# Kernel tuning notes

Measured on AMD Instinct MI355X. Metric: run time of the kernel, lower is better.

The kernel has to match this reference:

```python
import jax, jax.numpy as jnp
import numpy as np

EPS = 1e-6
B, C, T, F, K = 8, 128, 128, 512, 64


def conv1x1(x, w, b):
    # x: [B,C,H,W], w: [O,C], b: [O]
    return jnp.einsum('bcij,oc->boij', x, w) + b[None, :, None, None]


def rmsnorm(x, g):
    # RMSNorm over channel dim with per-channel gain
    return x * jax.lax.rsqrt(jnp.mean(x * x, axis=1, keepdims=True) + EPS) * g[None, :, None, None]


def swiglu(x, wi, bi, wo, bo):
    h = conv1x1(x, wi, bi)
    a, g = jnp.split(h, 2, axis=1)
    return conv1x1(a * jax.nn.silu(g), wo, bo)


def setup_inputs() -> dict:
    key = jax.random.key(0)
    ks = jax.random.split(key, 16)
    s = 1.0 / np.sqrt(C)
    # soft band-partition basis [K, F]: Gaussian bumps over frequency
    centers = np.linspace(0, F - 1, K)[:, None]
    freqs = np.arange(F)[None, :]
    basis = np.exp(-((freqs - centers) / (F / K)) ** 2).astype(np.float32)
    inp = {
        'latent': jax.random.normal(ks[0], (B, C, T, K), jnp.float32),
        'side': jax.random.normal(ks[1], (B, C, T, F), jnp.float32),
        'expansion_basis': jnp.asarray(basis),
        'lp_gamma': jnp.ones((C,), jnp.float32),
        'lp_w': jax.random.normal(ks[2], (C, C), jnp.float32) * s,
        'lp_b': jnp.zeros((C,), jnp.float32),
        'qn_gamma': jnp.ones((C,), jnp.float32),
        'qmlp_in_w': jax.random.normal(ks[3], (2 * C, C), jnp.float32) * s,
        'qmlp_in_b': jnp.zeros((2 * C,), jnp.float32),
        'qmlp_out_w': jax.random.normal(ks[4], (C, C), jnp.float32) * s,
        'qmlp_out_b': jnp.zeros((C,), jnp.float32),
        'q_w': jax.random.normal(ks[5], (C, C), jnp.float32) * s,
        'q_b': jnp.zeros((C,), jnp.float32),
        'k_w': jax.random.normal(ks[6], (C, C), jnp.float32) * s,
        'k_b': jnp.zeros((C,), jnp.float32),
        'v_w': jax.random.normal(ks[7], (C, C), jnp.float32) * s,
        'v_b': jnp.zeros((C,), jnp.float32),
        'o_w': jax.random.normal(ks[8], (C, C), jnp.float32) * s,
        'o_b': jnp.zeros((C,), jnp.float32),
        'ffn_gamma': jnp.ones((C,), jnp.float32),
        'ffn_in_w': jax.random.normal(ks[9], (2 * C, C), jnp.float32) * s,
        'ffn_in_b': jnp.zeros((2 * C,), jnp.float32),
        'ffn_out_w': jax.random.normal(ks[10], (C, C), jnp.float32) * s,
        'ffn_out_b': jnp.zeros((C,), jnp.float32),
        'score_scale': jnp.asarray(1.0 / np.sqrt(C), jnp.float32),
        'prior_scale': jnp.asarray(1.0, jnp.float32),
        'query_skip_scale': jnp.asarray(1.0, jnp.float32),
    }
    return inp


def reference(latent, side, expansion_basis, lp_gamma, lp_w, lp_b, qn_gamma,
              qmlp_in_w, qmlp_in_b, qmlp_out_w, qmlp_out_b,
              q_w, q_b, k_w, k_b, v_w, v_b, o_w, o_b,
              ffn_gamma, ffn_in_w, ffn_in_b, ffn_out_w, ffn_out_b,
              score_scale, prior_scale, query_skip_scale):
    # latent_pre: RMSNorm -> 1x1 conv -> SiLU   (latent: [B,C,T,K])
    latent_h = jax.nn.silu(conv1x1(rmsnorm(latent, lp_gamma), lp_w, lp_b))
    # adaptive query from full-resolution side path (side: [B,C,T,F])
    query_h = swiglu(rmsnorm(side, qn_gamma), qmlp_in_w, qmlp_in_b, qmlp_out_w, qmlp_out_b)
    # q/k/v projections (1x1 convs)
    q = conv1x1(query_h, q_w, q_b)      # [B,C,T,F]
    k = conv1x1(latent_h, k_w, k_b)     # [B,C,T,K]
    v = conv1x1(latent_h, v_w, v_b)     # [B,C,T,K]
    # per-frame cross-attention scores [B,T,F,K]
    scores = jnp.einsum('bctf,bctk->btfk', q, k) * score_scale
    # learned band-prior bias: expansion_basis [K,F] -> [F,K]
    scores = scores + expansion_basis.T[None, None] * prior_scale
    weights = jax.nn.softmax(scores, axis=-1)  # normalize_band_scores, mode='softmax'
    attended = jnp.einsum('btfk,bctk->bctf', weights, v)
    hidden = conv1x1(attended, o_w, o_b) + query_h * query_skip_scale
    hidden = hidden + swiglu(rmsnorm(hidden, ffn_gamma), ffn_in_w, ffn_in_b, ffn_out_w, ffn_out_b)
    return hidden  # [B,C,T,F]
```

## Files before the change

kernel.cpp:

```cpp
#include <hip/hip_runtime.h>

static constexpr int Cc = 128, Tt = 128, Ff = 512, Kk = 64;
static constexpr int SR = 136;
static constexpr int PR = 88;

typedef __bf16 bf16x8 __attribute__((ext_vector_type(8)));
typedef __bf16 bf16x4 __attribute__((ext_vector_type(4)));
typedef float f32x16 __attribute__((ext_vector_type(16)));
typedef float f32x4 __attribute__((ext_vector_type(4)));

__device__ __forceinline__ f32x16 z16() {
  f32x16 v;
#pragma unroll
  for (int i = 0; i < 16; ++i) v[i] = 0.f;
  return v;
}
__device__ __forceinline__ f32x4 z4() {
  f32x4 v;
#pragma unroll
  for (int i = 0; i < 4; ++i) v[i] = 0.f;
  return v;
}
__device__ __forceinline__ float silu_f(float x) { return x / (1.0f + __expf(-x)); }

__device__ __forceinline__ void rmsnorm_lds(const __bf16* __restrict__ src,
                                            __bf16* __restrict__ dst,
                                            const float* __restrict__ gamma,
                                            float* sPart, float* sr, int tid) {
  {
    int f = tid >> 2, s2 = tid & 3;
    const __bf16* p = src + f * SR + s2 * 32;
    float sum = 0.f;
#pragma unroll
    for (int k = 0; k < 4; ++k) {
      bf16x8 v = *(const bf16x8*)(p + k * 8);
#pragma unroll
      for (int j = 0; j < 8; ++j) { float x = (float)v[j]; sum += x * x; }
    }
    sPart[f * 4 + s2] = sum;
  }
  __syncthreads();
  if (tid < 64) {
    float s = sPart[tid * 4] + sPart[tid * 4 + 1] + sPart[tid * 4 + 2] + sPart[tid * 4 + 3];
    sr[tid] = rsqrtf(s * (1.f / 128.f) + 1e-6f);
  }
  __syncthreads();
#pragma unroll
  for (int i = 0; i < 32; ++i) {
    int idx = i * 256 + tid;
    int f = idx >> 7, c = idx & 127;
    dst[f * SR + c] = (__bf16)((float)src[f * SR + c] * sr[f] * gamma[c]);
  }
}

template <typename EPI>
__device__ __forceinline__ void unit_std(const __bf16* __restrict__ X,
                                         const __bf16* __restrict__ W,
                                         int lane, int wave, EPI epi) {
  const int h = lane >> 5, ol = lane & 31;
  const int p = wave >> 1, mt = wave & 1;
  const int oA = p * 64 + ol;
  bf16x8 B0[8], B1[8];
#pragma unroll
  for (int s = 0; s < 8; ++s) {
    B0[s] = *(const bf16x8*)(W + (size_t)oA * 128 + s * 16 + h * 8);
    B1[s] = *(const bf16x8*)(W + (size_t)(oA + 32) * 128 + s * 16 + h * 8);
  }
  f32x16 a0 = z16(), a1 = z16();
  const __bf16* Ar = X + (mt * 32 + ol) * SR + h * 8;
#pragma unroll
  for (int s = 0; s < 8; ++s) {
    bf16x8 Af = *(const bf16x8*)(Ar + s * 16);
    a0 = __builtin_amdgcn_mfma_f32_32x32x16_bf16(Af, B0[s], a0, 0, 0, 0);
    a1 = __builtin_amdgcn_mfma_f32_32x32x16_bf16(Af, B1[s], a1, 0, 0, 0);
  }
  epi(a0, 0);
  epi(a1, 1);
}

struct PrepArgs {
  const float* src[9];
  int n[9];
};
__global__ __launch_bounds__(256) void prep_kernel(PrepArgs pa, __bf16* __restrict__ dst) {
  int off = 0;
  for (int m = 0; m < 9; ++m) {
    const float* s = pa.src[m];
    int n = pa.n[m];
    for (int i = blockIdx.x * 256 + threadIdx.x; i < n; i += gridDim.x * 256)
      dst[off + i] = (__bf16)s[i];
    off += n;
  }
}

__global__ __launch_bounds__(256, 2)
void kv_kernel(const float* __restrict__ latent, const float* __restrict__ lp_gamma,
               const float* __restrict__ lp_b, const float* __restrict__ k_b,
               const float* __restrict__ v_b,
               const __bf16* __restrict__ w_lp, const __bf16* __restrict__ w_k,
               const __bf16* __restrict__ w_v,
               __bf16* __restrict__ kbuf, __bf16* __restrict__ vbuf) {
  __shared__ __align__(16) __bf16 S0[64 * SR];
  __shared__ __align__(16) __bf16 S1[64 * SR];
  __shared__ float sPart[256];
  __shared__ float sr[64];
  const int tid = threadIdx.x;
  const int lane = tid & 63, wave = tid >> 6;
  const int h = lane >> 5, ol = lane & 31;
  const int fr = blockIdx.x;
  const int b = fr >> 7, t = fr & 127;
  const size_t lbase = ((size_t)b * Cc * Tt + t) * Kk;

#pragma unroll
  for (int i = 0; i < 32; ++i) {
    int idx = i * 256 + tid;
    int c = idx >> 6, kk = idx & 63;
    S0[kk * SR + c] = (__bf16)latent[lbase + (size_t)c * Tt * Kk + kk];
  }
  __syncthreads();
  rmsnorm_lds(S0, S0, lp_gamma, sPart, sr, tid);
  __syncthreads();

  unit_std(S0, w_lp, lane, wave, [&](const f32x16& a, int tix) {
    int o = (wave >> 1) * 64 + tix * 32 + ol;
    int mt = wave & 1;
    float bb = lp_b[o];
#pragma unroll
    for (int r = 0; r < 16; ++r) {
      int f = mt * 32 + (r & 3) + 8 * (r >> 2) + 4 * h;
      S1[f * SR + o] = (__bf16)silu_f(a[r] + bb);
    }
  });
  __syncthreads();

  __bf16* kb = kbuf + (size_t)fr * 8192;
  unit_std(S1, w_k, lane, wave, [&](const f32x16& a, int tix) {
    int o = (wave >> 1) * 64 + tix * 32 + ol;
    int mt = wave & 1;
    float bb = k_b[o];
#pragma unroll
    for (int r = 0; r < 16; ++r) {
      int kkr = mt * 32 + (r & 3) + 8 * (r >> 2) + 4 * h;
      kb[kkr * 128 + o] = (__bf16)(a[r] + bb);
    }
  });
  __bf16* vb = vbuf + (size_t)fr * 8192;
  unit_std(S1, w_v, lane, wave, [&](const f32x16& a, int tix) {
    int o = (wave >> 1) * 64 + tix * 32 + ol;
    int mt = wave & 1;
    float bb = v_b[o];
    __bf16* vbo = vb + (size_t)o * 64 + mt * 32;
#pragma unroll
    for (int q = 0; q < 4; ++q) {
      bf16x4 pk;
      pk[0] = (__bf16)(a[4 * q + 0] + bb);
      pk[1] = (__bf16)(a[4 * q + 1] + bb);
      pk[2] = (__bf16)(a[4 * q + 2] + bb);
      pk[3] = (__bf16)(a[4 * q + 3] + bb);
      *(bf16x4*)(vbo + 8 * q + 4 * h) = pk;
    }
  });
}

__global__ __launch_bounds__(256, 2)
void main_kernel(const float* __restrict__ side, const float* __restrict__ basis,
                 const float* __restrict__ qn_gamma,
                 const float* __restrict__ qin_b, const float* __restrict__ qout_b,
                 const float* __restrict__ q_b, const float* __restrict__ o_b,
                 const float* __restrict__ ffn_gamma,
                 const float* __restrict__ fin_b, const float* __restrict__ fout_b,
                 const __bf16* __restrict__ w_qin, const __bf16* __restrict__ w_qout,
                 const __bf16* __restrict__ w_q, const __bf16* __restrict__ w_o,
                 const __bf16* __restrict__ w_fin, const __bf16* __restrict__ w_fout,
                 const __bf16* __restrict__ kbuf, const __bf16* __restrict__ vbuf,
                 const float* __restrict__ p_sscale, const float* __restrict__ p_pscale,
                 const float* __restrict__ p_skip, float* __restrict__ out) {
  __shared__ __align__(16) __bf16 S0[64 * SR];
  __shared__ __align__(16) __bf16 S1[64 * SR];
  __shared__ __align__(16) __bf16 S2[64 * SR];
  __shared__ __align__(16) __bf16 PM[64 * PR];
  __shared__ float sPart[256];
  __shared__ float sr[64];
  const int tid = threadIdx.x;
  const int lane = tid & 63, wave = tid >> 6;
  const int h = lane >> 5, ol = lane & 31;
  const int bid = blockIdx.x;
  const int fr = bid >> 3, tile = bid & 7;
  const int b = fr >> 7, t = fr & 127;
  const int fbase = tile * 64;
  const size_t sbase = ((size_t)b * Cc * Tt + t) * Ff + fbase;
  const float sscale = *p_sscale, pscale = *p_pscale, skip = *p_skip;
  const __bf16* kfr = kbuf + (size_t)fr * 8192;
  const __bf16* vfr = vbuf + (size_t)fr * 8192;

#pragma unroll
  for (int i = 0; i < 32; ++i) {
    int idx = i * 256 + tid;
    int c = idx >> 6, f = idx & 63;
    S0[f * SR + c] = (__bf16)side[sbase + (size_t)c * Tt * Ff + f];
  }
  __syncthreads();
  rmsnorm_lds(S0, S0, qn_gamma, sPart, sr, tid);
  __syncthreads();

  {
    float sg[2][16];
    unit_std(S0, w_qin + 128 * 128, lane, wave, [&](const f32x16& a, int tix) {
      int o = (wave >> 1) * 64 + tix * 32 + ol;
      float bb = qin_b[128 + o];
#pragma unroll
      for (int r = 0; r < 16; ++r) sg[tix][r] = silu_f(a[r] + bb);
    });
    unit_std(S0, w_qin, lane, wave, [&](const f32x16& a, int tix) {
      int o = (wave >> 1) * 64 + tix * 32 + ol;
      int mt = wave & 1;
      float bb = qin_b[o];
#pragma unroll
      for (int r = 0; r < 16; ++r) {
        int f = mt * 32 + (r & 3) + 8 * (r >> 2) + 4 * h;
        S1[f * SR + o] = (__bf16)((a[r] + bb) * sg[tix][r]);
      }
    });
  }
  __syncthreads();

  unit_std(S1, w_qout, lane, wave, [&](const f32x16& a, int tix) {
    int o = (wave >> 1) * 64 + tix * 32 + ol;
    int mt = wave & 1;
    float bb = qout_b[o];
#pragma unroll
    for (int r = 0; r < 16; ++r) {
      int f = mt * 32 + (r & 3) + 8 * (r >> 2) + 4 * h;
      S2[f * SR + o] = (__bf16)(a[r] + bb);
    }
  });
  __syncthreads();

  unit_std(S2, w_q, lane, wave, [&](const f32x16& a, int tix) {
    int o = (wave >> 1) * 64 + tix * 32 + ol;
    int mt = wave & 1;
    float bb = q_b[o];
#pragma unroll
    for (int r = 0; r < 16; ++r) {
      int f = mt * 32 + (r & 3) + 8 * (r >> 2) + 4 * h;
      S0[f * SR + o] = (__bf16)(a[r] + bb);
    }
  });
  __syncthreads();

  {
    const int q4 = lane >> 4, li = lane & 15;
    const int fw = wave * 16;
    f32x4 acc[4] = {z4(), z4(), z4(), z4()};
    const __bf16* Ar = S0 + (fw + li) * SR + q4 * 8;
    const __bf16* Kr = kfr + li * 128 + q4 * 8;
#pragma unroll
    for (int s = 0; s < 4; ++s) {
      bf16x8 Af = *(const bf16x8*)(Ar + s * 32);
#pragma unroll
      for (int nt = 0; nt < 4; ++nt) {
        bf16x8 Bf = *(const bf16x8*)(Kr + nt * (16 * 128) + s * 32);
        acc[nt] = __builtin_amdgcn_mfma_f32_16x16x32_bf16(Af, Bf, acc[nt], 0, 0, 0);
      }
    }
    float sc[4][4];
#pragma unroll
    for (int nt = 0; nt < 4; ++nt)
#pragma unroll
      for (int r = 0; r < 4; ++r) {
        int kk = 16 * nt + li;
        int f = fw + 4 * q4 + r;
        sc[nt][r] = acc[nt][r] * sscale + pscale * basis[(size_t)kk * Ff + fbase + f];
      }
#pragma unroll
    for (int r = 0; r < 4; ++r) {
      float m = fmaxf(fmaxf(sc[0][r], sc[1][r]), fmaxf(sc[2][r], sc[3][r]));
      m = fmaxf(m, __shfl_xor(m, 1));
      m = fmaxf(m, __shfl_xor(m, 2));
      m = fmaxf(m, __shfl_xor(m, 4));
      m = fmaxf(m, __shfl_xor(m, 8));
      float e[4], ssum = 0.f;
#pragma unroll
      for (int nt = 0; nt < 4; ++nt) { e[nt] = __expf(sc[nt][r] - m); ssum += e[nt]; }
      ssum += __shfl_xor(ssum, 1);
      ssum += __shfl_xor(ssum, 2);
      ssum += __shfl_xor(ssum, 4);
      ssum += __shfl_xor(ssum, 8);
      float inv = 1.f / ssum;
      int f = fw + 4 * q4 + r;
#pragma unroll
      for (int nt = 0; nt < 4; ++nt) PM[f * PR + 16 * nt + li] = (__bf16)(e[nt] * inv);
    }
  }
  __syncthreads();

  {
    const __bf16* Vr = vfr + (size_t)(wave * 32 + ol) * 64 + h * 8;
    bf16x8 Bv[4];
#pragma unroll
    for (int s = 0; s < 4; ++s) Bv[s] = *(const bf16x8*)(Vr + s * 16);
    f32x16 a0 = z16(), a1 = z16();
    const __bf16* Ar = PM + ol * PR + h * 8;
#pragma unroll
    for (int s = 0; s < 4; ++s) {
      bf16x8 A0 = *(const bf16x8*)(Ar + s * 16);
      bf16x8 A1 = *(const bf16x8*)(Ar + 32 * PR + s * 16);
      a0 = __builtin_amdgcn_mfma_f32_32x32x16_bf16(A0, Bv[s], a0, 0, 0, 0);
      a1 = __builtin_amdgcn_mfma_f32_32x32x16_bf16(A1, Bv[s], a1, 0, 0, 0);
    }
    int c = wave * 32 + ol;
#pragma unroll
    for (int r = 0; r < 16; ++r) {
      int fl = (r & 3) + 8 * (r >> 2) + 4 * h;
      S1[fl * SR + c] = (__bf16)a0[r];
      S1[(32 + fl) * SR + c] = (__bf16)a1[r];
    }
  }
  __syncthreads();

  unit_std(S1, w_o, lane, wave, [&](const f32x16& a, int tix) {
    int o = (wave >> 1) * 64 + tix * 32 + ol;
    int mt = wave & 1;
    float bb = o_b[o];
#pragma unroll
    for (int r = 0; r < 16; ++r) {
      int f = mt * 32 + (r & 3) + 8 * (r >> 2) + 4 * h;
      S0[f * SR + o] = (__bf16)(a[r] + bb + skip * (float)S2[f * SR + o]);
    }
  });
  __syncthreads();

  rmsnorm_lds(S0, S2, ffn_gamma, sPart, sr, tid);
  __syncthreads();

  {
    float sg[2][16];
    unit_std(S2, w_fin + 128 * 128, lane, wave, [&](const f32x16& a, int tix) {
      int o = (wave >> 1) * 64 + tix * 32 + ol;
      float bb = fin_b[128 + o];
#pragma unroll
      for (int r = 0; r < 16; ++r) sg[tix][r] = silu_f(a[r] + bb);
    });
    unit_std(S2, w_fin, lane, wave, [&](const f32x16& a, int tix) {
      int o = (wave >> 1) * 64 + tix * 32 + ol;
      int mt = wave & 1;
      float bb = fin_b[o];
#pragma unroll
      for (int r = 0; r < 16; ++r) {
        int f = mt * 32 + (r & 3) + 8 * (r >> 2) + 4 * h;
        S1[f * SR + o] = (__bf16)((a[r] + bb) * sg[tix][r]);
      }
    });
  }
  __syncthreads();

  unit_std(S1, w_fout, lane, wave, [&](const f32x16& a, int tix) {
    int o = (wave >> 1) * 64 + tix * 32 + ol;
    int mt = wave & 1;
    float bb = fout_b[o];
    float* op = out + (((size_t)b * 128 + o) * 128 + t) * 512 + fbase + mt * 32;
#pragma unroll
    for (int q = 0; q < 4; ++q) {
      int f0l = 8 * q + 4 * h;
      float4 v;
      v.x = a[4 * q + 0] + bb + (float)S0[(mt * 32 + f0l + 0) * SR + o];
      v.y = a[4 * q + 1] + bb + (float)S0[(mt * 32 + f0l + 1) * SR + o];
      v.z = a[4 * q + 2] + bb + (float)S0[(mt * 32 + f0l + 2) * SR + o];
      v.w = a[4 * q + 3] + bb + (float)S0[(mt * 32 + f0l + 3) * SR + o];
      *(float4*)(op + f0l) = v;
    }
  });
}

extern "C" void kernel_launch(void* const* d_in, const int* in_sizes, int n_in,
                              void* d_out, int out_size, void* d_ws, size_t ws_size,
                              hipStream_t stream) {
  const float* latent    = (const float*)d_in[0];
  const float* side      = (const float*)d_in[1];
  const float* basis     = (const float*)d_in[2];
  const float* lp_gamma  = (const float*)d_in[3];
  const float* lp_w      = (const float*)d_in[4];
  const float* lp_b      = (const float*)d_in[5];
  const float* qn_gamma  = (const float*)d_in[6];
  const float* qin_w     = (const float*)d_in[7];
  const float* qin_b     = (const float*)d_in[8];
  const float* qout_w    = (const float*)d_in[9];
  const float* qout_b    = (const float*)d_in[10];
  const float* q_w       = (const float*)d_in[11];
  const float* q_b       = (const float*)d_in[12];
  const float* k_w       = (const float*)d_in[13];
  const float* k_b       = (const float*)d_in[14];
  const float* v_w       = (const float*)d_in[15];
  const float* v_b       = (const float*)d_in[16];
  const float* o_w       = (const float*)d_in[17];
  const float* o_b       = (const float*)d_in[18];
  const float* ffn_gamma = (const float*)d_in[19];
  const float* fin_w     = (const float*)d_in[20];
  const float* fin_b     = (const float*)d_in[21];
  const float* fout_w    = (const float*)d_in[22];
  const float* fout_b    = (const float*)d_in[23];
  const float* sscale    = (const float*)d_in[24];
  const float* pscale    = (const float*)d_in[25];
  const float* skipsc    = (const float*)d_in[26];

  __bf16* wsb = (__bf16*)d_ws;
  __bf16* kbuf = wsb;
  __bf16* vbuf = wsb + (size_t)1024 * 8192;
  __bf16* wbase = wsb + (size_t)2048 * 8192;
  __bf16* w_lp   = wbase;
  __bf16* w_qin  = w_lp + 16384;
  __bf16* w_qout = w_qin + 32768;
  __bf16* w_q    = w_qout + 16384;
  __bf16* w_k    = w_q + 16384;
  __bf16* w_v    = w_k + 16384;
  __bf16* w_o    = w_v + 16384;
  __bf16* w_fin  = w_o + 16384;
  __bf16* w_fout = w_fin + 32768;

  PrepArgs pa;
  pa.src[0] = lp_w;   pa.n[0] = 16384;
  pa.src[1] = qin_w;  pa.n[1] = 32768;
  pa.src[2] = qout_w; pa.n[2] = 16384;
  pa.src[3] = q_w;    pa.n[3] = 16384;
  pa.src[4] = k_w;    pa.n[4] = 16384;
  pa.src[5] = v_w;    pa.n[5] = 16384;
  pa.src[6] = o_w;    pa.n[6] = 16384;
  pa.src[7] = fin_w;  pa.n[7] = 32768;
  pa.src[8] = fout_w; pa.n[8] = 16384;

  prep_kernel<<<dim3(64), dim3(256), 0, stream>>>(pa, wbase);
  kv_kernel<<<dim3(1024), dim3(256), 0, stream>>>(
      latent, lp_gamma, lp_b, k_b, v_b, w_lp, w_k, w_v, kbuf, vbuf);
  main_kernel<<<dim3(8192), dim3(256), 0, stream>>>(
      side, basis, qn_gamma, qin_b, qout_b, q_b, o_b, ffn_gamma, fin_b, fout_b,
      w_qin, w_qout, w_q, w_o, w_fin, w_fout, kbuf, vbuf,
      sscale, pscale, skipsc, (float*)d_out);
}
```

Baseline: 1.110 ms.

## Shrink LDS footprint and use shuffle-based RMSNorm to raise occupancy

RMSNorm now keeps each thread's slice in registers and reduces across the four threads of a row with xor shuffles, removing two barriers and the sPart/sr scratch arrays. The main kernel aliases the PM score buffer onto S1 and rotates S0/S1 roles in the later stages, so LDS use per block drops. Launch bounds rise to 3 blocks per CU for main and 4 for kv, aiming at higher occupancy to hide memory latency. The cost is tighter register budgets, which may cause spills, and buffer aliasing that depends on barrier ordering being correct.

```diff
diff --git a/kernel.cpp b/kernel.cpp
--- a/kernel.cpp
+++ b/kernel.cpp
@@ -25,31 +25,28 @@
 
 __device__ __forceinline__ void rmsnorm_lds(const __bf16* __restrict__ src,
                                             __bf16* __restrict__ dst,
-                                            const float* __restrict__ gamma,
-                                            float* sPart, float* sr, int tid) {
-  {
-    int f = tid >> 2, s2 = tid & 3;
-    const __bf16* p = src + f * SR + s2 * 32;
-    float sum = 0.f;
-#pragma unroll
-    for (int k = 0; k < 4; ++k) {
-      bf16x8 v = *(const bf16x8*)(p + k * 8);
-#pragma unroll
-      for (int j = 0; j < 8; ++j) { float x = (float)v[j]; sum += x * x; }
-    }
-    sPart[f * 4 + s2] = sum;
-  }
-  __syncthreads();
-  if (tid < 64) {
-    float s = sPart[tid * 4] + sPart[tid * 4 + 1] + sPart[tid * 4 + 2] + sPart[tid * 4 + 3];
-    sr[tid] = rsqrtf(s * (1.f / 128.f) + 1e-6f);
-  }
-  __syncthreads();
-#pragma unroll
-  for (int i = 0; i < 32; ++i) {
-    int idx = i * 256 + tid;
-    int f = idx >> 7, c = idx & 127;
-    dst[f * SR + c] = (__bf16)((float)src[f * SR + c] * sr[f] * gamma[c]);
+                                            const float* __restrict__ gamma, int tid) {
+  const int f = tid >> 2, s2 = tid & 3;
+  const __bf16* p = src + f * SR + s2 * 32;
+  bf16x8 v[4];
+  float sum = 0.f;
+#pragma unroll
+  for (int k = 0; k < 4; ++k) {
+    v[k] = *(const bf16x8*)(p + k * 8);
+#pragma unroll
+    for (int j = 0; j < 8; ++j) { float x = (float)v[k][j]; sum += x * x; }
+  }
+  sum += __shfl_xor(sum, 1);
+  sum += __shfl_xor(sum, 2);
+  const float r = rsqrtf(sum * (1.f / 128.f) + 1e-6f);
+  __bf16* q = dst + f * SR + s2 * 32;
+#pragma unroll
+  for (int k = 0; k < 4; ++k) {
+    bf16x8 w;
+#pragma unroll
+    for (int j = 0; j < 8; ++j)
+      w[j] = (__bf16)((float)v[k][j] * r * gamma[s2 * 32 + k * 8 + j]);
+    *(bf16x8*)(q + k * 8) = w;
   }
 }
 
@@ -93,7 +90,7 @@
   }
 }
 
-__global__ __launch_bounds__(256, 2)
+__global__ __launch_bounds__(256, 4)
 void kv_kernel(const float* __restrict__ latent, const float* __restrict__ lp_gamma,
                const float* __restrict__ lp_b, const float* __restrict__ k_b,
                const float* __restrict__ v_b,
@@ -102,8 +99,6 @@
                __bf16* __restrict__ kbuf, __bf16* __restrict__ vbuf) {
   __shared__ __align__(16) __bf16 S0[64 * SR];
   __shared__ __align__(16) __bf16 S1[64 * SR];
-  __shared__ float sPart[256];
-  __shared__ float sr[64];
   const int tid = threadIdx.x;
   const int lane = tid & 63, wave = tid >> 6;
   const int h = lane >> 5, ol = lane & 31;
@@ -118,7 +113,7 @@
     S0[kk * SR + c] = (__bf16)latent[lbase + (size_t)c * Tt * Kk + kk];
   }
   __syncthreads();
-  rmsnorm_lds(S0, S0, lp_gamma, sPart, sr, tid);
+  rmsnorm_lds(S0, S0, lp_gamma, tid);
   __syncthreads();
 
   unit_std(S0, w_lp, lane, wave, [&](const f32x16& a, int tix) {
@@ -162,7 +157,7 @@
   });
 }
 
-__global__ __launch_bounds__(256, 2)
+__global__ __launch_bounds__(256, 3)
 void main_kernel(const float* __restrict__ side, const float* __restrict__ basis,
                  const float* __restrict__ qn_gamma,
                  const float* __restrict__ qin_b, const float* __restrict__ qout_b,
@@ -178,9 +173,7 @@
   __shared__ __align__(16) __bf16 S0[64 * SR];
   __shared__ __align__(16) __bf16 S1[64 * SR];
   __shared__ __align__(16) __bf16 S2[64 * SR];
-  __shared__ __align__(16) __bf16 PM[64 * PR];
-  __shared__ float sPart[256];
-  __shared__ float sr[64];
+  __bf16* const PM = S1;
   const int tid = threadIdx.x;
   const int lane = tid & 63, wave = tid >> 6;
   const int h = lane >> 5, ol = lane & 31;
@@ -200,7 +193,7 @@
     S0[f * SR + c] = (__bf16)side[sbase + (size_t)c * Tt * Ff + f];
   }
   __syncthreads();
-  rmsnorm_lds(S0, S0, qn_gamma, sPart, sr, tid);
+  rmsnorm_lds(S0, S0, qn_gamma, tid);
   __syncthreads();
 
   {
@@ -312,25 +305,25 @@
 #pragma unroll
     for (int r = 0; r < 16; ++r) {
       int fl = (r & 3) + 8 * (r >> 2) + 4 * h;
-      S1[fl * SR + c] = (__bf16)a0[r];
-      S1[(32 + fl) * SR + c] = (__bf16)a1[r];
-    }
-  }
-  __syncthreads();
-
-  unit_std(S1, w_o, lane, wave, [&](const f32x16& a, int tix) {
+      S0[fl * SR + c] = (__bf16)a0[r];
+      S0[(32 + fl) * SR + c] = (__bf16)a1[r];
+    }
+  }
+  __syncthreads();
+
+  unit_std(S0, w_o, lane, wave, [&](const f32x16& a, int tix) {
     int o = (wave >> 1) * 64 + tix * 32 + ol;
     int mt = wave & 1;
     float bb = o_b[o];
 #pragma unroll
     for (int r = 0; r < 16; ++r) {
       int f = mt * 32 + (r & 3) + 8 * (r >> 2) + 4 * h;
-      S0[f * SR + o] = (__bf16)(a[r] + bb + skip * (float)S2[f * SR + o]);
-    }
-  });
-  __syncthreads();
-
-  rmsnorm_lds(S0, S2, ffn_gamma, sPart, sr, tid);
+      S1[f * SR + o] = (__bf16)(a[r] + bb + skip * (float)S2[f * SR + o]);
+    }
+  });
+  __syncthreads();
+
+  rmsnorm_lds(S1, S2, ffn_gamma, tid);
   __syncthreads();
 
   {
@@ -348,13 +341,13 @@
 #pragma unroll
       for (int r = 0; r < 16; ++r) {
         int f = mt * 32 + (r & 3) + 8 * (r >> 2) + 4 * h;
-        S1[f * SR + o] = (__bf16)((a[r] + bb) * sg[tix][r]);
+        S0[f * SR + o] = (__bf16)((a[r] + bb) * sg[tix][r]);
       }
     });
   }
   __syncthreads();
 
-  unit_std(S1, w_fout, lane, wave, [&](const f32x16& a, int tix) {
+  unit_std(S0, w_fout, lane, wave, [&](const f32x16& a, int tix) {
     int o = (wave >> 1) * 64 + tix * 32 + ol;
     int mt = wave & 1;
     float bb = fout_b[o];
@@ -363,10 +356,10 @@
     for (int q = 0; q < 4; ++q) {
       int f0l = 8 * q + 4 * h;
       float4 v;
-      v.x = a[4 * q + 0] + bb + (float)S0[(mt * 32 + f0l + 0) * SR + o];
-      v.y = a[4 * q + 1] + bb + (float)S0[(mt * 32 + f0l + 1) * SR + o];
-      v.z = a[4 * q + 2] + bb + (float)S0[(mt * 32 + f0l + 2) * SR + o];
-      v.w = a[4 * q + 3] + bb + (float)S0[(mt * 32 + f0l + 3) * SR + o];
+      v.x = a[4 * q + 0] + bb + (float)S1[(mt * 32 + f0l + 0) * SR + o];
+      v.y = a[4 * q + 1] + bb + (float)S1[(mt * 32 + f0l + 1) * SR + o];
+      v.z = a[4 * q + 2] + bb + (float)S1[(mt * 32 + f0l + 2) * SR + o];
+      v.w = a[4 * q + 3] + bb + (float)S1[(mt * 32 + f0l + 3) * SR + o];
       *(float4*)(op + f0l) = v;
     }
   });
```

After: 1.101 ms. About the same (-0.8%).
